# Optimization experiments

Hardware: AMD Instinct MI355X
Metric: run time of the kernel (lower is better)

## Reference

```python
import jax, jax.numpy as jnp
import numpy as np


def l2_normalize(x, axis, eps=1e-12):
    # matches tf.nn.l2_normalize / K.l2_normalize
    return x * jax.lax.rsqrt(jnp.maximum(jnp.sum(x * x, axis=axis, keepdims=True), eps))


def setup_inputs() -> dict:
    key = jax.random.key(0)
    k1, k2 = jax.random.split(key)
    B, H, W, C = 32, 1, 900, 256
    return {
        "input_1": jax.random.normal(k1, (B, H, W, C), dtype=jnp.float32),
        "input_2": jax.random.normal(k2, (B, H, W, C), dtype=jnp.float32),
    }


def reference(input_1, input_2):
    B, H, W, C = input_1.shape
    p = W // 2
    # 'euclidean' normalization along the width (azimuth) axis, axis=2
    x1 = l2_normalize(input_1, axis=2)
    x2 = l2_normalize(input_2, axis=2)
    # RangePadding2D: circular padding along width to width 2W-1, so that a
    # VALID correlation with a W-wide kernel yields exactly W circular shifts.
    x1p = jnp.concatenate([x1[:, :, p:, :], x1, x1[:, :, : p - 1, :]], axis=2)  # [B,H,2W-1,C]
    # Per-sample correlation: out[b, j] = sum_{h,i,c} x1p[b,h,j+i,c] * x2[b,h,i,c]
    # Expressed as one grouped conv (one group per batch element) instead of tf.scan.
    lhs = jnp.transpose(x1p, (0, 3, 1, 2)).reshape(1, B * C, H, 2 * W - 1)  # NCHW
    rhs = jnp.transpose(x2, (0, 3, 1, 2))  # [B, C, H, W] OIHW
    out = jax.lax.conv_general_dilated(
        lhs, rhs,
        window_strides=(1, 1), padding="VALID",
        dimension_numbers=("NCHW", "OIHW", "NCHW"),
        feature_group_count=B,
    )  # [1, B, 1, W]
    # -> (B, H=1, W, output_dim=1), matching compute_output_shape
    return jnp.transpose(out, (1, 2, 3, 0))
```

## Files before the change

kernel.cpp:

```cpp
#include <hip/hip_runtime.h>
#include <hip/hip_bf16.h>

#define BATCH 32
#define WW 900
#define CCH 256
#define PVAL 450
#define KHALF 128
#define MSTRIP 128
#define NCHUNK 32
#define NCHUNKS 29

typedef __bf16 bf16x8 __attribute__((ext_vector_type(8)));
typedef __bf16 bf16x4 __attribute__((ext_vector_type(4)));
typedef float f32x4 __attribute__((ext_vector_type(4)));

#define INV15_OFF 245760
#define INV4_OFF  65536

__global__ void nc_norm_partial(const float* __restrict__ x1,
                                const float* __restrict__ x2,
                                float* __restrict__ sums,
                                float* __restrict__ out, int out_n,
                                int segs, int rowsper) {
    int blk = blockIdx.x;
    int oz = blk * 256 + threadIdx.x;
    if (oz < out_n) out[oz] = 0.f;
    int seg = blk % segs;
    int b = (blk / segs) & 31;
    int which = blk / (segs * 32);
    const float* x = which ? x2 : x1;
    int c = threadIdx.x;
    int r0 = seg * rowsper;
    int r1 = r0 + rowsper;
    if (r1 > WW) r1 = WW;
    const float* p = x + ((size_t)b * WW + r0) * CCH + c;
    float s = 0.f;
    #pragma unroll 4
    for (int w = 0; w < r1 - r0; ++w) {
        float v = p[(size_t)w * CCH];
        s = fmaf(v, v, s);
    }
    sums[(((size_t)(which * 32 + b)) * segs + seg) * CCH + c] = s;
}

template <int SEGS>
__global__ void nc_norm_finalize(float* __restrict__ ws, float* __restrict__ inv) {
    int i = blockIdx.x * 256 + threadIdx.x;
    int c = i & 255;
    int wb = i >> 8;
    const float* s = ws + (size_t)wb * SEGS * CCH + c;
    float t = 0.f;
    #pragma unroll
    for (int q = 0; q < SEGS; ++q) t += s[(size_t)q * CCH];
    inv[i] = rsqrtf(fmaxf(t, 1e-12f));
}

__global__ __launch_bounds__(256, 2)
void nc_corr(const float* __restrict__ x1,
             const float* __restrict__ x2,
             const float* __restrict__ invp,
             float* __restrict__ out) {
    __shared__ __bf16 Abuf[MSTRIP * KHALF];
    __shared__ __bf16 Bbuf[2][NCHUNK * KHALF];
    __shared__ float scratch[4][16][65];
    __shared__ float diag[2][4][64];
    __shared__ float partial[WW];

    const int tid = threadIdx.x;
    const int b = blockIdx.x & 31;
    const int strip = (blockIdx.x >> 5) & 7;
    const int kh = blockIdx.x >> 8;
    const int m0 = strip * MSTRIP;
    const int k0 = kh * KHALF;

    const float* __restrict__ inv1 = invp + b * CCH + k0;
    const float* __restrict__ inv2 = invp + (BATCH + b) * CCH + k0;
    const float* __restrict__ x1b = x1 + (size_t)b * WW * CCH + k0;
    const float* __restrict__ x2b = x2 + (size_t)b * WW * CCH + k0;

    for (int i = tid; i < WW; i += 256) partial[i] = 0.f;
    for (int i = tid; i < 4 * 16 * 65; i += 256) ((float*)scratch)[i] = 0.f;

    const int lane = tid & 63;
    const int wave = tid >> 6;
    const int fr = lane & 15;
    const int fq = lane >> 4;

    const int sr = tid >> 5;
    const int sg = tid & 31;

    {
        float4 iv1 = *(const float4*)(inv1 + sg * 4);
        #pragma unroll
        for (int k = 0; k < 16; ++k) {
            const int row = sr + 8 * k;
            const int m = m0 + row;
            float4 f = make_float4(0.f, 0.f, 0.f, 0.f);
            if (m < WW) f = *(const float4*)(x1b + (size_t)m * CCH + sg * 4);
            bf16x4 v = { (__bf16)(f.x * iv1.x), (__bf16)(f.y * iv1.y),
                         (__bf16)(f.z * iv1.z), (__bf16)(f.w * iv1.w) };
            *(bf16x4*)(&Abuf[row * KHALF + (((sg >> 1) ^ (row & 7)) << 3) + (sg & 1) * 4]) = v;
        }
    }

    const float4 ivB = *(const float4*)(inv2 + sg * 4);
    float4 st[4];

    auto loadB = [&](int chunk) {
        #pragma unroll
        for (int k = 0; k < 4; ++k) {
            const int row = chunk * NCHUNK + sr + 8 * k;
            st[k] = (row < WW) ? *(const float4*)(x2b + (size_t)row * CCH + sg * 4)
                               : make_float4(0.f, 0.f, 0.f, 0.f);
        }
    };
    auto writeB = [&](int buf) {
        #pragma unroll
        for (int k = 0; k < 4; ++k) {
            const int row = sr + 8 * k;
            float4 f = st[k];
            bf16x4 v = { (__bf16)(f.x * ivB.x), (__bf16)(f.y * ivB.y),
                         (__bf16)(f.z * ivB.z), (__bf16)(f.w * ivB.w) };
            *(bf16x4*)(&Bbuf[buf][row * KHALF + (((sg >> 1) ^ (row & 7)) << 3) + (sg & 1) * 4]) = v;
        }
    };

    loadB(0);
    writeB(0);
    __syncthreads();

    bf16x8 afm[2][4];
    #pragma unroll
    for (int mt = 0; mt < 2; ++mt)
        #pragma unroll
        for (int kk = 0; kk < 4; ++kk) {
            const int row = wave * 32 + mt * 16 + fr;
            const int g = (kk * 4 + fq) ^ (row & 7);
            afm[mt][kk] = *(const bf16x8*)(&Abuf[row * KHALF + g * 8]);
        }
    #pragma unroll
    for (int mt = 0; mt < 2; ++mt)
        #pragma unroll
        for (int kk = 0; kk < 4; ++kk)
            asm volatile("" : "+v"(afm[mt][kk]));

    int cur = 0;
    for (int chunk = 0; chunk < NCHUNKS; ++chunk) {
        if (chunk + 1 < NCHUNKS) {
            loadB(chunk + 1);
            __builtin_amdgcn_sched_barrier(0);
        }

        f32x4 acc[2][2];
        #pragma unroll
        for (int mt = 0; mt < 2; ++mt)
            #pragma unroll
            for (int nt = 0; nt < 2; ++nt)
                acc[mt][nt] = (f32x4){0.f, 0.f, 0.f, 0.f};

        #pragma unroll
        for (int kk = 0; kk < 4; ++kk) {
            bf16x8 bfr[2];
            #pragma unroll
            for (int nt = 0; nt < 2; ++nt) {
                const int row = nt * 16 + fr;
                const int g = (kk * 4 + fq) ^ (row & 7);
                bfr[nt] = *(const bf16x8*)(&Bbuf[cur][row * KHALF + g * 8]);
            }
            #pragma unroll
            for (int mt = 0; mt < 2; ++mt)
                #pragma unroll
                for (int nt = 0; nt < 2; ++nt)
                    acc[mt][nt] = __builtin_amdgcn_mfma_f32_16x16x32_bf16(
                        afm[mt][kk], bfr[nt], acc[mt][nt], 0, 0, 0);
        }

        {
            f32x4 c0 = acc[0][1];
            f32x4 c1 = acc[0][0] + acc[1][1];
            f32x4 c2 = acc[1][0];
            const int mub = 4 * fq;
            #pragma unroll
            for (int r = 0; r < 4; ++r) {
                const int mu = mub + r;
                const int dr = mu - fr + 15;
                scratch[wave][mu][dr]      = c0[r];
                scratch[wave][mu][dr + 16] = c1[r];
                scratch[wave][mu][dr + 32] = c2[r];
            }
        }

        {
            float s = 0.f;
            #pragma unroll
            for (int m = 0; m < 16; ++m) s += scratch[wave][m][lane];
            diag[chunk & 1][wave][lane] = s;
        }

        if (chunk + 1 < NCHUNKS) writeB(cur ^ 1);
        __syncthreads();

        if (tid < 159) {
            float s = 0.f;
            #pragma unroll
            for (int w = 0; w < 4; ++w) {
                const int dr = tid - 32 * w;
                if (dr >= 0 && dr < 63) s += diag[chunk & 1][w][dr];
            }
            int v = m0 - 32 * chunk + tid + 1319;
            if (v >= 1800) v -= 900;
            if (v >= 900) v -= 900;
            partial[v] += s;
        }
        cur ^= 1;
    }

    __syncthreads();
    for (int i = tid; i < WW; i += 256)
        unsafeAtomicAdd(&out[(size_t)b * WW + i], partial[i]);
}

extern "C" void kernel_launch(void* const* d_in, const int* in_sizes, int n_in,
                              void* d_out, int out_size, void* d_ws, size_t ws_size,
                              hipStream_t stream) {
    const float* x1 = (const float*)d_in[0];
    const float* x2 = (const float*)d_in[1];
    float* out = (float*)d_out;
    float* ws = (float*)d_ws;

    const size_t need15 = (size_t)(INV15_OFF + 16384) * sizeof(float);
    if (ws_size >= need15) {
        const int segs = 15, rowsper = 60;
        nc_norm_partial<<<2 * 32 * segs, 256, 0, stream>>>(x1, x2, ws, out, out_size, segs, rowsper);
        nc_norm_finalize<15><<<64, 256, 0, stream>>>(ws, ws + INV15_OFF);
        nc_corr<<<512, 256, 0, stream>>>(x1, x2, ws + INV15_OFF, out);
    } else {
        const int segs = 4, rowsper = 225;
        nc_norm_partial<<<2 * 32 * segs, 256, 0, stream>>>(x1, x2, ws, out, out_size, segs, rowsper);
        nc_norm_finalize<4><<<64, 256, 0, stream>>>(ws, ws + INV4_OFF);
        nc_corr<<<512, 256, 0, stream>>>(x1, x2, ws + INV4_OFF, out);
    }
}
```

Baseline: 55.20 us.

## Double the B chunk to 64 rows and alias diagonal scratch onto A buffer

Each pipeline step now loads 64 rows of x2 per chunk instead of 32, so the loop runs 15 times instead of 29. Each step issues twice as many MFMAs, and the diagonal reduction handles five 16-wide bands instead of three. This is meant to halve the barriers and per-chunk overhead. The scratch area now reuses the A staging buffer after the A fragments are in registers, which frees LDS to make room for the larger B buffers. The first B load is also issued before the A tile is staged so the two loads overlap. In exchange each thread uses more registers for staging and accumulators, which may hurt occupancy under launch_bounds(256,2).

```diff
diff --git a/kernel.cpp b/kernel.cpp
--- a/kernel.cpp
+++ b/kernel.cpp
@@ -7,8 +7,8 @@
 #define PVAL 450
 #define KHALF 128
 #define MSTRIP 128
-#define NCHUNK 32
-#define NCHUNKS 29
+#define NCHUNK 64
+#define NCHUNKS 15
 
 typedef __bf16 bf16x8 __attribute__((ext_vector_type(8)));
 typedef __bf16 bf16x4 __attribute__((ext_vector_type(4)));
@@ -62,9 +62,10 @@
              float* __restrict__ out) {
     __shared__ __bf16 Abuf[MSTRIP * KHALF];
     __shared__ __bf16 Bbuf[2][NCHUNK * KHALF];
-    __shared__ float scratch[4][16][65];
-    __shared__ float diag[2][4][64];
+    __shared__ float diag[2][4][96];
     __shared__ float partial[WW];
+
+    float (*scratch)[16][97] = (float (*)[16][97])Abuf;
 
     const int tid = threadIdx.x;
     const int b = blockIdx.x & 31;
@@ -78,9 +79,6 @@
     const float* __restrict__ x1b = x1 + (size_t)b * WW * CCH + k0;
     const float* __restrict__ x2b = x2 + (size_t)b * WW * CCH + k0;
 
-    for (int i = tid; i < WW; i += 256) partial[i] = 0.f;
-    for (int i = tid; i < 4 * 16 * 65; i += 256) ((float*)scratch)[i] = 0.f;
-
     const int lane = tid & 63;
     const int wave = tid >> 6;
     const int fr = lane & 15;
@@ -88,6 +86,30 @@
 
     const int sr = tid >> 5;
     const int sg = tid & 31;
+
+    const float4 ivB = *(const float4*)(inv2 + sg * 4);
+    float4 st[8];
+
+    auto loadB = [&](int chunk) {
+        #pragma unroll
+        for (int k = 0; k < 8; ++k) {
+            const int row = chunk * NCHUNK + sr + 8 * k;
+            st[k] = (row < WW) ? *(const float4*)(x2b + (size_t)row * CCH + sg * 4)
+                               : make_float4(0.f, 0.f, 0.f, 0.f);
+        }
+    };
+    auto writeB = [&](int buf) {
+        #pragma unroll
+        for (int k = 0; k < 8; ++k) {
+            const int row = sr + 8 * k;
+            float4 f = st[k];
+            bf16x4 v = { (__bf16)(f.x * ivB.x), (__bf16)(f.y * ivB.y),
+                         (__bf16)(f.z * ivB.z), (__bf16)(f.w * ivB.w) };
+            *(bf16x4*)(&Bbuf[buf][row * KHALF + (((sg >> 1) ^ sr) << 3) + (sg & 1) * 4]) = v;
+        }
+    };
+
+    loadB(0);
 
     {
         float4 iv1 = *(const float4*)(inv1 + sg * 4);
@@ -103,29 +125,7 @@
         }
     }
 
-    const float4 ivB = *(const float4*)(inv2 + sg * 4);
-    float4 st[4];
-
-    auto loadB = [&](int chunk) {
-        #pragma unroll
-        for (int k = 0; k < 4; ++k) {
-            const int row = chunk * NCHUNK + sr + 8 * k;
-            st[k] = (row < WW) ? *(const float4*)(x2b + (size_t)row * CCH + sg * 4)
-                               : make_float4(0.f, 0.f, 0.f, 0.f);
-        }
-    };
-    auto writeB = [&](int buf) {
-        #pragma unroll
-        for (int k = 0; k < 4; ++k) {
-            const int row = sr + 8 * k;
-            float4 f = st[k];
-            bf16x4 v = { (__bf16)(f.x * ivB.x), (__bf16)(f.y * ivB.y),
-                         (__bf16)(f.z * ivB.z), (__bf16)(f.w * ivB.w) };
-            *(bf16x4*)(&Bbuf[buf][row * KHALF + (((sg >> 1) ^ (row & 7)) << 3) + (sg & 1) * 4]) = v;
-        }
-    };
-
-    loadB(0);
+    for (int i = tid; i < WW; i += 256) partial[i] = 0.f;
     writeB(0);
     __syncthreads();
 
@@ -143,6 +143,13 @@
         #pragma unroll
         for (int kk = 0; kk < 4; ++kk)
             asm volatile("" : "+v"(afm[mt][kk]));
+
+    __syncthreads();
+
+    {
+        float* sw = (float*)&scratch[wave][0][0];
+        for (int i = lane; i < 16 * 97; i += 64) sw[i] = 0.f;
+    }
 
     int cur = 0;
     for (int chunk = 0; chunk < NCHUNKS; ++chunk) {
@@ -151,18 +158,18 @@
             __builtin_amdgcn_sched_barrier(0);
         }
 
-        f32x4 acc[2][2];
+        f32x4 acc[2][4];
         #pragma unroll
         for (int mt = 0; mt < 2; ++mt)
             #pragma unroll
-            for (int nt = 0; nt < 2; ++nt)
+            for (int nt = 0; nt < 4; ++nt)
                 acc[mt][nt] = (f32x4){0.f, 0.f, 0.f, 0.f};
 
         #pragma unroll
         for (int kk = 0; kk < 4; ++kk) {
-            bf16x8 bfr[2];
-            #pragma unroll
-            for (int nt = 0; nt < 2; ++nt) {
+            bf16x8 bfr[4];
+            #pragma unroll
+            for (int nt = 0; nt < 4; ++nt) {
                 const int row = nt * 16 + fr;
                 const int g = (kk * 4 + fq) ^ (row & 7);
                 bfr[nt] = *(const bf16x8*)(&Bbuf[cur][row * KHALF + g * 8]);
@@ -170,23 +177,27 @@
             #pragma unroll
             for (int mt = 0; mt < 2; ++mt)
                 #pragma unroll
-                for (int nt = 0; nt < 2; ++nt)
+                for (int nt = 0; nt < 4; ++nt)
                     acc[mt][nt] = __builtin_amdgcn_mfma_f32_16x16x32_bf16(
                         afm[mt][kk], bfr[nt], acc[mt][nt], 0, 0, 0);
         }
 
         {
-            f32x4 c0 = acc[0][1];
-            f32x4 c1 = acc[0][0] + acc[1][1];
-            f32x4 c2 = acc[1][0];
+            f32x4 c0 = acc[0][3];
+            f32x4 c1 = acc[0][2] + acc[1][3];
+            f32x4 c2 = acc[0][1] + acc[1][2];
+            f32x4 c3 = acc[0][0] + acc[1][1];
+            f32x4 c4 = acc[1][0];
             const int mub = 4 * fq;
             #pragma unroll
             for (int r = 0; r < 4; ++r) {
                 const int mu = mub + r;
-                const int dr = mu - fr + 15;
-                scratch[wave][mu][dr]      = c0[r];
-                scratch[wave][mu][dr + 16] = c1[r];
-                scratch[wave][mu][dr + 32] = c2[r];
+                const int drb = mu - fr + 15;
+                scratch[wave][mu][drb]      = c0[r];
+                scratch[wave][mu][drb + 16] = c1[r];
+                scratch[wave][mu][drb + 32] = c2[r];
+                scratch[wave][mu][drb + 48] = c3[r];
+                scratch[wave][mu][drb + 64] = c4[r];
             }
         }
 
@@ -195,19 +206,25 @@
             #pragma unroll
             for (int m = 0; m < 16; ++m) s += scratch[wave][m][lane];
             diag[chunk & 1][wave][lane] = s;
+            if (lane < 31) {
+                float s2 = 0.f;
+                #pragma unroll
+                for (int m = 0; m < 16; ++m) s2 += scratch[wave][m][64 + lane];
+                diag[chunk & 1][wave][64 + lane] = s2;
+            }
         }
 
         if (chunk + 1 < NCHUNKS) writeB(cur ^ 1);
         __syncthreads();
 
-        if (tid < 159) {
+        if (tid < 191) {
             float s = 0.f;
             #pragma unroll
             for (int w = 0; w < 4; ++w) {
                 const int dr = tid - 32 * w;
-                if (dr >= 0 && dr < 63) s += diag[chunk & 1][w][dr];
-            }
-            int v = m0 - 32 * chunk + tid + 1319;
+                if (dr >= 0 && dr < 95) s += diag[chunk & 1][w][dr];
+            }
+            int v = m0 - 64 * chunk + tid + 1287;
             if (v >= 1800) v -= 900;
             if (v >= 900) v -= 900;
             partial[v] += s;
```

After: 50.59 us. 1.09x faster.
